# Kernel optimization log

Measured on AMD Instinct MI355X. Metric: run time of the kernel, lower is better.

The kernel has to match this reference:

```python
import jax, jax.numpy as jnp
import numpy as np

T, N, D, H = 128, 512, 1024, 1024
LN_EPS = 1e-5


def setup_inputs() -> dict:
    key = jax.random.key(0)
    ks = jax.random.split(key, 6)
    x = jax.random.normal(ks[0], (T * N, D), jnp.float32)
    hxs = jax.random.normal(ks[1], (N, 1, H), jnp.float32)
    # binary done-masks (float, mostly 1.0 = keep hidden state, 0.0 = episode reset)
    masks = (jax.random.uniform(ks[2], (T * N, 1)) < 0.95).astype(jnp.float32)
    s = 1.0 / np.sqrt(H)
    # PyTorch GRU packed gates, order (r, z, n): weight_ih_l0 [3H, D], weight_hh_l0 [3H, H]
    W_ih = jax.random.normal(ks[3], (3 * H, D), jnp.float32) * s
    W_hh = jax.random.normal(ks[4], (3 * H, H), jnp.float32) * s
    b_ih = jnp.zeros((3 * H,), jnp.float32)  # module inits biases to 0
    b_hh = jnp.zeros((3 * H,), jnp.float32)
    gamma = jnp.ones((H,), jnp.float32)
    beta = jnp.zeros((H,), jnp.float32)
    return dict(x=x, hxs=hxs, masks=masks, W_ih=W_ih, W_hh=W_hh,
                b_ih=b_ih, b_hh=b_hh, gamma=gamma, beta=beta)


def reference(x, hxs, masks, W_ih, W_hh, b_ih, b_hh, gamma, beta):
    TN = x.shape[0]
    Nn = hxs.shape[0]
    Tt = TN // Nn
    Hd = hxs.shape[-1]
    xs = x.reshape(Tt, Nn, -1)          # [T, N, D]
    m = masks.reshape(Tt, Nn)           # [T, N]
    # Chunk starts per source: t=0 plus every t>=1 where (masks[t] == 1).any().
    # At a chunk start the hidden state is multiplied by masks[t] (broadcast over layers);
    # a scan with a per-step conditional mask-multiply is exactly equivalent to the
    # torch loop over chunks.
    reset = jnp.concatenate([jnp.ones((1,), bool), jnp.any(m[1:] == 1.0, axis=-1)])
    # Batch the input projection across all T*N tokens (one big GEMM): [T, N, 3H]
    xp = jnp.einsum('tnd,gd->tng', xs, W_ih) + b_ih
    h0 = hxs[:, 0, :]                   # recurrent_N == 1 -> [N, H]

    def step(h, inp):
        xp_t, m_t, r_t = inp
        h = jnp.where(r_t, h * m_t[:, None], h)
        hp = h @ W_hh.T + b_hh          # [N, 3H]
        xr, xz, xn = jnp.split(xp_t, 3, axis=-1)
        hr, hz, hn = jnp.split(hp, 3, axis=-1)
        r = jax.nn.sigmoid(xr + hr)
        z = jax.nn.sigmoid(xz + hz)
        n = jnp.tanh(xn + r * hn)
        h_new = (1.0 - z) * n + z * h
        return h_new, h_new

    h_last, outs = jax.lax.scan(step, h0, (xp, m, reset))
    y = outs.reshape(Tt * Nn, Hd)
    # LayerNorm over last dim
    mu = y.mean(-1, keepdims=True)
    var = y.var(-1, keepdims=True)
    y = (y - mu) * jax.lax.rsqrt(var + LN_EPS) * gamma + beta
    return y, h_last[:, None, :]
```

## Files before the change

### kernel.cpp

```cpp
#include <hip/hip_runtime.h>

#define T_STEPS 128
#define N_B     512
#define D_IN    1024
#define H_DIM   1024
#define G_DIM   3072
#define M_ALL   (T_STEPS * N_B)

typedef short          s8v  __attribute__((ext_vector_type(8)));
typedef float          f4v  __attribute__((ext_vector_type(4)));
typedef unsigned short u4v  __attribute__((ext_vector_type(4)));

__device__ __forceinline__ unsigned short f2bf(float f) {
  union { float f; unsigned u; } v; v.f = f;
  unsigned r = v.u + 0x7FFFu + ((v.u >> 16) & 1u);
  return (unsigned short)(r >> 16);
}
__device__ __forceinline__ float bf2f(unsigned short h) {
  union { unsigned u; float f; } v; v.u = ((unsigned)h) << 16;
  return v.f;
}
__device__ __forceinline__ void async16(const void* g, void* l) {
  __builtin_amdgcn_global_load_lds(
      (const __attribute__((address_space(1))) unsigned*)g,
      (__attribute__((address_space(3))) unsigned*)l, 16, 0, 0);
}
__device__ __forceinline__ float sigmoidf_(float x) { return 1.f / (1.f + __expf(-x)); }
__device__ __forceinline__ float tanhf_(float x)    { return 1.f - 2.f / (1.f + __expf(2.f * x)); }

__global__ void cvt_bf16(const float* __restrict__ in, unsigned short* __restrict__ out, long n4) {
  long i = (long)blockIdx.x * blockDim.x + threadIdx.x;
  long stride = (long)gridDim.x * blockDim.x;
  for (; i < n4; i += stride) {
    f4v v = *(const f4v*)(in + i * 4);
    u4v o;
    #pragma unroll
    for (int e = 0; e < 4; ++e) o[e] = f2bf(v[e]);
    *(u4v*)(out + i * 4) = o;
  }
}

__global__ void reset_kernel(const float* __restrict__ masks, int* __restrict__ reset) {
  const int t = blockIdx.x;
  __shared__ int flag;
  if (threadIdx.x == 0) flag = (t == 0) ? 1 : 0;
  __syncthreads();
  if (t > 0 && masks[(size_t)t * N_B + threadIdx.x] == 1.0f) flag = 1;
  __syncthreads();
  if (threadIdx.x == 0) reset[t] = flag;
}

__global__ __launch_bounds__(256) void gemm_xp(const unsigned short* __restrict__ A,
                                               const unsigned short* __restrict__ B,
                                               const float* __restrict__ bias,
                                               unsigned short* __restrict__ C) {
  const int m0 = blockIdx.y * 128, g0 = blockIdx.x * 128;
  const int tid = threadIdx.x, wv = tid >> 6, l = tid & 63;
  const int l15 = l & 15, l4 = l >> 4;
  const int wr = wv >> 1, wc = wv & 1;
  __shared__ unsigned short As[128 * 64], Bs[128 * 64];

  f4v zero4 = {0.f, 0.f, 0.f, 0.f};
  f4v acc[4][4];
  #pragma unroll
  for (int i = 0; i < 4; ++i)
    #pragma unroll
    for (int j = 0; j < 4; ++j) acc[i][j] = zero4;

  const int srow = l >> 3;
  const int selem = ((l & 7) ^ srow) * 8;
  const int swz_rd = (l15 & 7) << 4;

  for (int kt = 0; kt < 1024; kt += 64) {
    #pragma unroll
    for (int cc = 0; cc < 4; ++cc) {
      int s = wv * 4 + cc;
      int row = s * 8 + srow;
      async16(A + (size_t)(m0 + row) * 1024 + kt + selem, &As[s * 512]);
      async16(B + (size_t)(g0 + row) * 1024 + kt + selem, &Bs[s * 512]);
    }
    __syncthreads();
    #pragma unroll
    for (int ks = 0; ks < 2; ++ks) {
      s8v a[4], b[4];
      #pragma unroll
      for (int i = 0; i < 4; ++i) {
        int ra = wr * 64 + i * 16 + l15, rb = wc * 64 + i * 16 + l15;
        int cb = (ks * 64 + l4 * 16) ^ swz_rd;
        a[i] = *(const s8v*)((const char*)As + ra * 128 + cb);
        b[i] = *(const s8v*)((const char*)Bs + rb * 128 + cb);
      }
      #pragma unroll
      for (int i = 0; i < 4; ++i)
        #pragma unroll
        for (int j = 0; j < 4; ++j)
          acc[i][j] = __builtin_amdgcn_mfma_f32_16x16x32_bf16(a[i], b[j], acc[i][j], 0, 0, 0);
    }
    __syncthreads();
  }
  #pragma unroll
  for (int j = 0; j < 4; ++j) {
    int gcol = g0 + wc * 64 + j * 16 + l15;
    float bv = bias[gcol];
    #pragma unroll
    for (int i = 0; i < 4; ++i) {
      int mrow = m0 + wr * 64 + i * 16 + l4 * 4;
      u4v o;
      #pragma unroll
      for (int r = 0; r < 4; ++r) o[r] = f2bf(acc[i][j][r] + bv);
      *(u4v*)(C + (size_t)gcol * M_ALL + mrow) = o;
    }
  }
}

__global__ __launch_bounds__(256) void gru_step7(
    const unsigned short* __restrict__ Whh,
    const unsigned short* __restrict__ xpT,
    const float* __restrict__ masks,
    const int* __restrict__ reset,
    const float* __restrict__ bhh,
    const float* __restrict__ hxs,
    const unsigned short* __restrict__ hread,
    unsigned short* __restrict__ hwrite,
    const float* __restrict__ hf32r,
    float* __restrict__ hf32w,
    float* __restrict__ y,
    float* __restrict__ hlast,
    int t) {
  const int bid = blockIdx.x;
  const int jt = bid & 31, nt = bid >> 5;
  const int j0 = jt * 32, n0 = nt * 64;
  const int tid = threadIdx.x, w = tid >> 6, l = tid & 63;
  const int l15 = l & 15, l4 = l >> 4;
  const int wn = w & 1, wj = w >> 1;
  const size_t NH = (size_t)N_B * H_DIM;

  __shared__ unsigned short Hs[3][64 * 128];
  __shared__ unsigned short Ws[3][96 * 128];
  __shared__ unsigned short xpl[3][32][64];

  const int lrow4 = l >> 4;
  const int lcb = (l & 15) * 16;
  const int swz_rd = (l15 & 7) << 4;

  const int jj = j0 + wj * 16 + l15;
  const int rst = reset[t];

  bool zo[2];
  #pragma unroll
  for (int i = 0; i < 2; ++i) {
    float mv = masks[(size_t)t * N_B + n0 + wn * 32 + i * 16 + l15];
    zo[i] = rst && (mv == 0.0f);
  }
  const float* hsrc = (t == 0) ? hxs : hf32r;
  float hreg[2][4], mreg[2][4];
  #pragma unroll
  for (int i = 0; i < 2; ++i)
    #pragma unroll
    for (int r = 0; r < 4; ++r) {
      const int n = n0 + wn * 32 + i * 16 + l4 * 4 + r;
      hreg[i][r] = hsrc[(size_t)n * H_DIM + jj];
      mreg[i][r] = masks[(size_t)t * N_B + n];
    }
  const float br = bhh[jj];
  const float bz = bhh[H_DIM + jj];
  const float bn = bhh[2 * H_DIM + jj];

  f4v zero4 = {0.f, 0.f, 0.f, 0.f};
  s8v zer8 = {0, 0, 0, 0, 0, 0, 0, 0};
  f4v acc[2][3];
  #pragma unroll
  for (int i = 0; i < 2; ++i)
    #pragma unroll
    for (int g3 = 0; g3 < 3; ++g3) acc[i][g3] = zero4;

  auto stage = [&](int buf, int kt) {
    #pragma unroll
    for (int q = 0; q < 4; ++q) {
      int rb = w * 16 + q * 4;
      int row = rb + lrow4;
      int cb = lcb ^ ((row & 7) << 4);
      async16(hread + (size_t)(n0 + row) * H_DIM + kt * 128 + (cb >> 1), &Hs[buf][rb * 128]);
    }
    #pragma unroll
    for (int q = 0; q < 6; ++q) {
      int rb = w * 24 + q * 4;
      int row = rb + lrow4;
      int gate = row >> 5, jjl = row & 31;
      int cb = lcb ^ ((row & 7) << 4);
      async16(Whh + ((size_t)gate * H_DIM + j0 + jjl) * H_DIM + kt * 128 + (cb >> 1),
              &Ws[buf][rb * 128]);
    }
  };

  stage(0, 0); stage(1, 1); stage(2, 2);

  {
    const int jl = w * 8 + (l >> 3);
    const int nelem = ((l & 7) ^ (l >> 3)) * 8;
    #pragma unroll
    for (int g3 = 0; g3 < 3; ++g3)
      async16(xpT + (size_t)(g3 * H_DIM + j0 + jl) * M_ALL + (size_t)t * N_B + n0 + nelem,
              &xpl[g3][w * 8][0]);
  }

#define KT_BODY(KT, VM, DO_STAGE)                                              \
  {                                                                            \
    asm volatile("s_waitcnt vmcnt(" #VM ")" ::: "memory");                     \
    __builtin_amdgcn_s_barrier();                                              \
    __builtin_amdgcn_sched_barrier(0);                                         \
    if (DO_STAGE) stage((KT + 2) % 3, KT + 2);                                 \
    const char* hb = (const char*)&Hs[KT % 3][0];                              \
    const char* wb = (const char*)&Ws[KT % 3][0];                              \
    _Pragma("unroll")                                                          \
    for (int ks = 0; ks < 4; ++ks) {                                           \
      const int kbb = (ks * 64 + l4 * 16) ^ swz_rd;                            \
      s8v a[2], b[3];                                                          \
      _Pragma("unroll")                                                        \
      for (int i = 0; i < 2; ++i) {                                            \
        a[i] = *(const s8v*)(hb + (wn * 32 + i * 16 + l15) * 256 + kbb);       \
        if (zo[i]) a[i] = zer8;                                                \
      }                                                                        \
      _Pragma("unroll")                                                        \
      for (int g3 = 0; g3 < 3; ++g3)                                           \
        b[g3] = *(const s8v*)(wb + (g3 * 32 + wj * 16 + l15) * 256 + kbb);     \
      _Pragma("unroll")                                                        \
      for (int i = 0; i < 2; ++i)                                              \
        _Pragma("unroll")                                                      \
        for (int g3 = 0; g3 < 3; ++g3)                                         \
          acc[i][g3] = __builtin_amdgcn_mfma_f32_16x16x32_bf16(a[i], b[g3],    \
                                                              acc[i][g3], 0, 0, 0); \
    }                                                                          \
  }

  KT_BODY(0, 23, false)
  KT_BODY(1, 13, true)
  KT_BODY(2, 13, true)
  KT_BODY(3, 10, true)
  KT_BODY(4, 10, true)
  KT_BODY(5, 10, true)
  KT_BODY(6, 10, false)
  KT_BODY(7, 0,  false)
#undef KT_BODY

  #pragma unroll
  for (int i = 0; i < 2; ++i) {
    #pragma unroll
    for (int r = 0; r < 4; ++r) {
      const int n = n0 + wn * 32 + i * 16 + l4 * 4 + r;
      const int nl = wn * 32 + i * 16 + l4 * 4 + r;
      const int jl = wj * 16 + l15;
      float hprev = hreg[i][r];
      if (rst && mreg[i][r] == 0.0f) hprev = 0.0f;
      const float hr = acc[i][0][r] + br;
      const float hz = acc[i][1][r] + bz;
      const float hn = acc[i][2][r] + bn;
      const char* xb = (const char*)&xpl[0][0][0];
      const int nb = (nl * 2) ^ ((jl & 7) << 4);
      const float xr = bf2f(*(const unsigned short*)(xb + 0 * 4096 + jl * 128 + nb));
      const float xz = bf2f(*(const unsigned short*)(xb + 1 * 4096 + jl * 128 + nb));
      const float xn = bf2f(*(const unsigned short*)(xb + 2 * 4096 + jl * 128 + nb));
      const float rg = sigmoidf_(xr + hr);
      const float zg = sigmoidf_(xz + hz);
      const float ng = tanhf_(xn + rg * hn);
      const float hnew = (1.f - zg) * ng + zg * hprev;
      const size_t gidx = (size_t)n * H_DIM + jj;
      y[(size_t)t * NH + gidx] = hnew;
      hwrite[gidx] = f2bf(hnew);
      hf32w[gidx] = hnew;
      if (t == T_STEPS - 1) hlast[gidx] = hnew;
    }
  }
}

__global__ __launch_bounds__(256) void ln_kernel(float* __restrict__ y,
                                                 const float* __restrict__ gamma,
                                                 const float* __restrict__ beta) {
  const size_t row = blockIdx.x;
  float* p = y + row * (size_t)H_DIM;
  const int tid = threadIdx.x;
  f4v v = *(const f4v*)(p + tid * 4);
  float s = v[0] + v[1] + v[2] + v[3];
  float q = v[0] * v[0] + v[1] * v[1] + v[2] * v[2] + v[3] * v[3];
  #pragma unroll
  for (int off = 32; off > 0; off >>= 1) {
    s += __shfl_down(s, off);
    q += __shfl_down(q, off);
  }
  __shared__ float sb[8];
  const int wid = tid >> 6, lid = tid & 63;
  if (lid == 0) { sb[wid] = s; sb[4 + wid] = q; }
  __syncthreads();
  float S = sb[0] + sb[1] + sb[2] + sb[3];
  float Q = sb[4] + sb[5] + sb[6] + sb[7];
  float mean = S * (1.f / H_DIM);
  float var = Q * (1.f / H_DIM) - mean * mean;
  float inv = rsqrtf(var + 1e-5f);
  f4v g4 = *(const f4v*)(gamma + tid * 4);
  f4v b4 = *(const f4v*)(beta + tid * 4);
  f4v o;
  #pragma unroll
  for (int e = 0; e < 4; ++e) o[e] = (v[e] - mean) * inv * g4[e] + b4[e];
  *(f4v*)(p + tid * 4) = o;
}

extern "C" void kernel_launch(void* const* d_in, const int* in_sizes, int n_in,
                              void* d_out, int out_size, void* d_ws, size_t ws_size,
                              hipStream_t stream) {
  const float* x     = (const float*)d_in[0];
  const float* hxs   = (const float*)d_in[1];
  const float* masks = (const float*)d_in[2];
  const float* W_ih  = (const float*)d_in[3];
  const float* W_hh  = (const float*)d_in[4];
  const float* b_ih  = (const float*)d_in[5];
  const float* b_hh  = (const float*)d_in[6];
  const float* gamma = (const float*)d_in[7];
  const float* beta  = (const float*)d_in[8];
  float* y = (float*)d_out;
  float* hlast = y + (size_t)T_STEPS * N_B * H_DIM;

  char* ws = (char*)d_ws;
  unsigned short* Wih_bf = (unsigned short*)ws;  ws += (size_t)G_DIM * D_IN * 2;
  unsigned short* Whh_bf = (unsigned short*)ws;  ws += (size_t)G_DIM * H_DIM * 2;
  unsigned short* xc_bf  = (unsigned short*)ws;  ws += (size_t)M_ALL * D_IN * 2;
  unsigned short* xpT_bf = (unsigned short*)ws;  ws += (size_t)G_DIM * M_ALL * 2;
  unsigned short* hbuf   = (unsigned short*)ws;  ws += (size_t)2 * N_B * H_DIM * 2;
  float* hf32            = (float*)ws;           ws += (size_t)2 * N_B * H_DIM * 4;
  int* reset             = (int*)ws;             ws += 512;

  cvt_bf16<<<1024, 256, 0, stream>>>(W_ih, Wih_bf, (long)G_DIM * D_IN / 4);
  cvt_bf16<<<1024, 256, 0, stream>>>(W_hh, Whh_bf, (long)G_DIM * H_DIM / 4);
  cvt_bf16<<<512, 256, 0, stream>>>(hxs, hbuf, (long)N_B * H_DIM / 4);
  reset_kernel<<<128, 512, 0, stream>>>(masks, reset);
  cvt_bf16<<<4096, 256, 0, stream>>>(x, xc_bf, (long)M_ALL * D_IN / 4);

  dim3 gg(G_DIM / 128, M_ALL / 128);
  gemm_xp<<<gg, 256, 0, stream>>>(xc_bf, Wih_bf, b_ih, xpT_bf);

  const size_t NH = (size_t)N_B * H_DIM;
  for (int t = 0; t < T_STEPS; ++t) {
    const unsigned short* hread = hbuf + (size_t)(t & 1) * NH;
    unsigned short* hwrite = hbuf + (size_t)((t & 1) ^ 1) * NH;
    const float* hf32r = hf32 + (size_t)(t & 1) * NH;
    float* hf32w = hf32 + (size_t)((t & 1) ^ 1) * NH;
    gru_step7<<<256, 256, 0, stream>>>(Whh_bf, xpT_bf, masks, reset, b_hh,
                                       hxs, hread, hwrite, hf32r, hf32w, y, hlast, t);
  }

  ln_kernel<<<T_STEPS * N_B, 256, 0, stream>>>(y, gamma, beta);
}
```

Baseline: 2.483 ms.

## Fuse GRU time steps into one persistent kernel with per-group grid barriers

Replaces the 128 per-timestep launches with a single persistent kernel that loops over time. Each block keeps its fp32 hidden slice in registers, and the blocks sharing a batch group synchronise through an atomic counter barrier. The aim is to remove per-step launch overhead and the fp32 hidden-state round trip through global memory. The kernel needs all 256 blocks to be co-resident, or the barrier can deadlock. The bf16 hidden loads use a cache-bypass flag so that other blocks' writes are visible, but the barrier uses relaxed atomics with no explicit fences, so cross-block ordering is a risk.

```diff
diff --git a/kernel.cpp b/kernel.cpp
--- a/kernel.cpp
+++ b/kernel.cpp
@@ -6,6 +6,7 @@
 #define H_DIM   1024
 #define G_DIM   3072
 #define M_ALL   (T_STEPS * N_B)
+#define BAR_STRIDE 64
 
 typedef short          s8v  __attribute__((ext_vector_type(8)));
 typedef float          f4v  __attribute__((ext_vector_type(4)));
@@ -24,6 +25,11 @@
   __builtin_amdgcn_global_load_lds(
       (const __attribute__((address_space(1))) unsigned*)g,
       (__attribute__((address_space(3))) unsigned*)l, 16, 0, 0);
+}
+__device__ __forceinline__ void async16_sc0(const void* g, void* l) {
+  __builtin_amdgcn_global_load_lds(
+      (const __attribute__((address_space(1))) unsigned*)g,
+      (__attribute__((address_space(3))) unsigned*)l, 16, 0, 1);
 }
 __device__ __forceinline__ float sigmoidf_(float x) { return 1.f / (1.f + __expf(-x)); }
 __device__ __forceinline__ float tanhf_(float x)    { return 1.f - 2.f / (1.f + __expf(2.f * x)); }
@@ -113,23 +119,20 @@
   }
 }
 
-__global__ __launch_bounds__(256) void gru_step7(
+__global__ __launch_bounds__(256) void rnn_chunk6(
     const unsigned short* __restrict__ Whh,
     const unsigned short* __restrict__ xpT,
     const float* __restrict__ masks,
     const int* __restrict__ reset,
     const float* __restrict__ bhh,
     const float* __restrict__ hxs,
-    const unsigned short* __restrict__ hread,
-    unsigned short* __restrict__ hwrite,
-    const float* __restrict__ hf32r,
-    float* __restrict__ hf32w,
+    unsigned short* hbuf,
     float* __restrict__ y,
     float* __restrict__ hlast,
-    int t) {
+    unsigned* bar) {
   const int bid = blockIdx.x;
-  const int jt = bid & 31, nt = bid >> 5;
-  const int j0 = jt * 32, n0 = nt * 64;
+  const int g = bid & 7, c = bid >> 3;
+  const int n0 = g * 64, j0 = c * 32;
   const int tid = threadIdx.x, w = tid >> 6, l = tid & 63;
   const int l15 = l & 15, l4 = l >> 4;
   const int wn = w & 1, wj = w >> 1;
@@ -144,132 +147,151 @@
   const int swz_rd = (l15 & 7) << 4;
 
   const int jj = j0 + wj * 16 + l15;
-  const int rst = reset[t];
-
-  bool zo[2];
-  #pragma unroll
-  for (int i = 0; i < 2; ++i) {
-    float mv = masks[(size_t)t * N_B + n0 + wn * 32 + i * 16 + l15];
-    zo[i] = rst && (mv == 0.0f);
-  }
-  const float* hsrc = (t == 0) ? hxs : hf32r;
-  float hreg[2][4], mreg[2][4];
-  #pragma unroll
-  for (int i = 0; i < 2; ++i)
-    #pragma unroll
-    for (int r = 0; r < 4; ++r) {
-      const int n = n0 + wn * 32 + i * 16 + l4 * 4 + r;
-      hreg[i][r] = hsrc[(size_t)n * H_DIM + jj];
-      mreg[i][r] = masks[(size_t)t * N_B + n];
-    }
   const float br = bhh[jj];
   const float bz = bhh[H_DIM + jj];
   const float bn = bhh[2 * H_DIM + jj];
 
+  float hreg[2][4];
+  #pragma unroll
+  for (int i = 0; i < 2; ++i)
+    #pragma unroll
+    for (int r = 0; r < 4; ++r)
+      hreg[i][r] = hxs[(size_t)(n0 + wn * 32 + i * 16 + l4 * 4 + r) * H_DIM + jj];
+
   f4v zero4 = {0.f, 0.f, 0.f, 0.f};
   s8v zer8 = {0, 0, 0, 0, 0, 0, 0, 0};
-  f4v acc[2][3];
-  #pragma unroll
-  for (int i = 0; i < 2; ++i)
-    #pragma unroll
-    for (int g3 = 0; g3 < 3; ++g3) acc[i][g3] = zero4;
-
-  auto stage = [&](int buf, int kt) {
-    #pragma unroll
-    for (int q = 0; q < 4; ++q) {
-      int rb = w * 16 + q * 4;
-      int row = rb + lrow4;
-      int cb = lcb ^ ((row & 7) << 4);
-      async16(hread + (size_t)(n0 + row) * H_DIM + kt * 128 + (cb >> 1), &Hs[buf][rb * 128]);
-    }
-    #pragma unroll
-    for (int q = 0; q < 6; ++q) {
-      int rb = w * 24 + q * 4;
-      int row = rb + lrow4;
-      int gate = row >> 5, jjl = row & 31;
-      int cb = lcb ^ ((row & 7) << 4);
-      async16(Whh + ((size_t)gate * H_DIM + j0 + jjl) * H_DIM + kt * 128 + (cb >> 1),
-              &Ws[buf][rb * 128]);
-    }
-  };
-
-  stage(0, 0); stage(1, 1); stage(2, 2);
-
-  {
-    const int jl = w * 8 + (l >> 3);
-    const int nelem = ((l & 7) ^ (l >> 3)) * 8;
-    #pragma unroll
-    for (int g3 = 0; g3 < 3; ++g3)
-      async16(xpT + (size_t)(g3 * H_DIM + j0 + jl) * M_ALL + (size_t)t * N_B + n0 + nelem,
-              &xpl[g3][w * 8][0]);
-  }
+
+  for (int t = 0; t < T_STEPS; ++t) {
+    const unsigned short* hread = hbuf + (size_t)(t & 1) * NH;
+    unsigned short* hwrite = hbuf + (size_t)((t & 1) ^ 1) * NH;
+    const int rst = reset[t];
+
+    bool zo[2];
+    #pragma unroll
+    for (int i = 0; i < 2; ++i) {
+      float mv = masks[(size_t)t * N_B + n0 + wn * 32 + i * 16 + l15];
+      zo[i] = rst && (mv == 0.0f);
+    }
+    float mreg[2][4];
+    #pragma unroll
+    for (int i = 0; i < 2; ++i)
+      #pragma unroll
+      for (int r = 0; r < 4; ++r)
+        mreg[i][r] = masks[(size_t)t * N_B + n0 + wn * 32 + i * 16 + l4 * 4 + r];
+
+    f4v acc[2][3];
+    #pragma unroll
+    for (int i = 0; i < 2; ++i)
+      #pragma unroll
+      for (int g3 = 0; g3 < 3; ++g3) acc[i][g3] = zero4;
+
+    auto stage = [&](int buf, int kt) {
+      #pragma unroll
+      for (int q = 0; q < 4; ++q) {
+        int rb = w * 16 + q * 4;
+        int row = rb + lrow4;
+        int cb = lcb ^ ((row & 7) << 4);
+        async16_sc0(hread + (size_t)(n0 + row) * H_DIM + kt * 128 + (cb >> 1),
+                    &Hs[buf][rb * 128]);
+      }
+      #pragma unroll
+      for (int q = 0; q < 6; ++q) {
+        int rb = w * 24 + q * 4;
+        int row = rb + lrow4;
+        int gate = row >> 5, jjl = row & 31;
+        int cb = lcb ^ ((row & 7) << 4);
+        async16(Whh + ((size_t)gate * H_DIM + j0 + jjl) * H_DIM + kt * 128 + (cb >> 1),
+                &Ws[buf][rb * 128]);
+      }
+    };
+
+    stage(0, 0); stage(1, 1); stage(2, 2);
+
+    {
+      const int jl = w * 8 + (l >> 3);
+      const int nelem = ((l & 7) ^ (l >> 3)) * 8;
+      #pragma unroll
+      for (int g3 = 0; g3 < 3; ++g3)
+        async16(xpT + (size_t)(g3 * H_DIM + j0 + jl) * M_ALL + (size_t)t * N_B + n0 + nelem,
+                &xpl[g3][w * 8][0]);
+    }
 
 #define KT_BODY(KT, VM, DO_STAGE)                                              \
-  {                                                                            \
-    asm volatile("s_waitcnt vmcnt(" #VM ")" ::: "memory");                     \
-    __builtin_amdgcn_s_barrier();                                              \
-    __builtin_amdgcn_sched_barrier(0);                                         \
-    if (DO_STAGE) stage((KT + 2) % 3, KT + 2);                                 \
-    const char* hb = (const char*)&Hs[KT % 3][0];                              \
-    const char* wb = (const char*)&Ws[KT % 3][0];                              \
-    _Pragma("unroll")                                                          \
-    for (int ks = 0; ks < 4; ++ks) {                                           \
-      const int kbb = (ks * 64 + l4 * 16) ^ swz_rd;                            \
-      s8v a[2], b[3];                                                          \
+    {                                                                          \
+      asm volatile("s_waitcnt vmcnt(" #VM ")" ::: "memory");                   \
+      __builtin_amdgcn_s_barrier();                                            \
+      __builtin_amdgcn_sched_barrier(0);                                       \
+      if (DO_STAGE) stage((KT + 2) % 3, KT + 2);                               \
+      const char* hb = (const char*)&Hs[KT % 3][0];                            \
+      const char* wb = (const char*)&Ws[KT % 3][0];                            \
       _Pragma("unroll")                                                        \
-      for (int i = 0; i < 2; ++i) {                                            \
-        a[i] = *(const s8v*)(hb + (wn * 32 + i * 16 + l15) * 256 + kbb);       \
-        if (zo[i]) a[i] = zer8;                                                \
-      }                                                                        \
-      _Pragma("unroll")                                                        \
-      for (int g3 = 0; g3 < 3; ++g3)                                           \
-        b[g3] = *(const s8v*)(wb + (g3 * 32 + wj * 16 + l15) * 256 + kbb);     \
-      _Pragma("unroll")                                                        \
-      for (int i = 0; i < 2; ++i)                                              \
+      for (int ks = 0; ks < 4; ++ks) {                                         \
+        const int kbb = (ks * 64 + l4 * 16) ^ swz_rd;                          \
+        s8v a[2], b[3];                                                        \
+        _Pragma("unroll")                                                      \
+        for (int i = 0; i < 2; ++i) {                                          \
+          a[i] = *(const s8v*)(hb + (wn * 32 + i * 16 + l15) * 256 + kbb);     \
+          if (zo[i]) a[i] = zer8;                                              \
+        }                                                                      \
         _Pragma("unroll")                                                      \
         for (int g3 = 0; g3 < 3; ++g3)                                         \
-          acc[i][g3] = __builtin_amdgcn_mfma_f32_16x16x32_bf16(a[i], b[g3],    \
-                                                              acc[i][g3], 0, 0, 0); \
-    }                                                                          \
-  }
-
-  KT_BODY(0, 23, false)
-  KT_BODY(1, 13, true)
-  KT_BODY(2, 13, true)
-  KT_BODY(3, 10, true)
-  KT_BODY(4, 10, true)
-  KT_BODY(5, 10, true)
-  KT_BODY(6, 10, false)
-  KT_BODY(7, 0,  false)
+          b[g3] = *(const s8v*)(wb + (g3 * 32 + wj * 16 + l15) * 256 + kbb);   \
+        _Pragma("unroll")                                                      \
+        for (int i = 0; i < 2; ++i)                                            \
+          _Pragma("unroll")                                                    \
+          for (int g3 = 0; g3 < 3; ++g3)                                       \
+            acc[i][g3] = __builtin_amdgcn_mfma_f32_16x16x32_bf16(a[i], b[g3],  \
+                                                                acc[i][g3], 0, 0, 0); \
+      }                                                                        \
+    }
+
+    KT_BODY(0, 23, false)
+    KT_BODY(1, 13, true)
+    KT_BODY(2, 13, true)
+    KT_BODY(3, 10, true)
+    KT_BODY(4, 10, true)
+    KT_BODY(5, 10, true)
+    KT_BODY(6, 10, false)
+    KT_BODY(7, 0,  false)
 #undef KT_BODY
 
-  #pragma unroll
-  for (int i = 0; i < 2; ++i) {
-    #pragma unroll
-    for (int r = 0; r < 4; ++r) {
-      const int n = n0 + wn * 32 + i * 16 + l4 * 4 + r;
-      const int nl = wn * 32 + i * 16 + l4 * 4 + r;
-      const int jl = wj * 16 + l15;
-      float hprev = hreg[i][r];
-      if (rst && mreg[i][r] == 0.0f) hprev = 0.0f;
-      const float hr = acc[i][0][r] + br;
-      const float hz = acc[i][1][r] + bz;
-      const float hn = acc[i][2][r] + bn;
-      const char* xb = (const char*)&xpl[0][0][0];
-      const int nb = (nl * 2) ^ ((jl & 7) << 4);
-      const float xr = bf2f(*(const unsigned short*)(xb + 0 * 4096 + jl * 128 + nb));
-      const float xz = bf2f(*(const unsigned short*)(xb + 1 * 4096 + jl * 128 + nb));
-      const float xn = bf2f(*(const unsigned short*)(xb + 2 * 4096 + jl * 128 + nb));
-      const float rg = sigmoidf_(xr + hr);
-      const float zg = sigmoidf_(xz + hz);
-      const float ng = tanhf_(xn + rg * hn);
-      const float hnew = (1.f - zg) * ng + zg * hprev;
-      const size_t gidx = (size_t)n * H_DIM + jj;
-      y[(size_t)t * NH + gidx] = hnew;
-      hwrite[gidx] = f2bf(hnew);
-      hf32w[gidx] = hnew;
-      if (t == T_STEPS - 1) hlast[gidx] = hnew;
-    }
+    #pragma unroll
+    for (int i = 0; i < 2; ++i) {
+      #pragma unroll
+      for (int r = 0; r < 4; ++r) {
+        const int n = n0 + wn * 32 + i * 16 + l4 * 4 + r;
+        const int nl = wn * 32 + i * 16 + l4 * 4 + r;
+        const int jl = wj * 16 + l15;
+        float hprev = hreg[i][r];
+        if (rst && mreg[i][r] == 0.0f) hprev = 0.0f;
+        const float hr = acc[i][0][r] + br;
+        const float hz = acc[i][1][r] + bz;
+        const float hn = acc[i][2][r] + bn;
+        const char* xb = (const char*)&xpl[0][0][0];
+        const int nb = (nl * 2) ^ ((jl & 7) << 4);
+        const float xr = bf2f(*(const unsigned short*)(xb + 0 * 4096 + jl * 128 + nb));
+        const float xz = bf2f(*(const unsigned short*)(xb + 1 * 4096 + jl * 128 + nb));
+        const float xn = bf2f(*(const unsigned short*)(xb + 2 * 4096 + jl * 128 + nb));
+        const float rg = sigmoidf_(xr + hr);
+        const float zg = sigmoidf_(xz + hz);
+        const float ng = tanhf_(xn + rg * hn);
+        const float hnew = (1.f - zg) * ng + zg * hprev;
+        hreg[i][r] = hnew;
+        const size_t gidx = (size_t)n * H_DIM + jj;
+        y[(size_t)t * NH + gidx] = hnew;
+        hwrite[gidx] = f2bf(hnew);
+        if (t == T_STEPS - 1) hlast[gidx] = hnew;
+      }
+    }
+
+    __syncthreads();
+    if (tid == 0) {
+      __hip_atomic_fetch_add(&bar[g * BAR_STRIDE], 1u, __ATOMIC_RELAXED, __HIP_MEMORY_SCOPE_AGENT);
+      const unsigned tgt = 32u * (unsigned)(t + 1);
+      while (__hip_atomic_load(&bar[g * BAR_STRIDE], __ATOMIC_RELAXED, __HIP_MEMORY_SCOPE_AGENT) < tgt)
+        __builtin_amdgcn_s_sleep(1);
+    }
+    __syncthreads();
   }
 }
 
@@ -325,9 +347,10 @@
   unsigned short* xc_bf  = (unsigned short*)ws;  ws += (size_t)M_ALL * D_IN * 2;
   unsigned short* xpT_bf = (unsigned short*)ws;  ws += (size_t)G_DIM * M_ALL * 2;
   unsigned short* hbuf   = (unsigned short*)ws;  ws += (size_t)2 * N_B * H_DIM * 2;
-  float* hf32            = (float*)ws;           ws += (size_t)2 * N_B * H_DIM * 4;
+  unsigned* bars         = (unsigned*)ws;        ws += 8 * BAR_STRIDE * sizeof(unsigned);
   int* reset             = (int*)ws;             ws += 512;
 
+  hipMemsetAsync(bars, 0, 8 * BAR_STRIDE * sizeof(unsigned), stream);
   cvt_bf16<<<1024, 256, 0, stream>>>(W_ih, Wih_bf, (long)G_DIM * D_IN / 4);
   cvt_bf16<<<1024, 256, 0, stream>>>(W_hh, Whh_bf, (long)G_DIM * H_DIM / 4);
   cvt_bf16<<<512, 256, 0, stream>>>(hxs, hbuf, (long)N_B * H_DIM / 4);
@@ -337,15 +360,8 @@
   dim3 gg(G_DIM / 128, M_ALL / 128);
   gemm_xp<<<gg, 256, 0, stream>>>(xc_bf, Wih_bf, b_ih, xpT_bf);
 
-  const size_t NH = (size_t)N_B * H_DIM;
-  for (int t = 0; t < T_STEPS; ++t) {
-    const unsigned short* hread = hbuf + (size_t)(t & 1) * NH;
-    unsigned short* hwrite = hbuf + (size_t)((t & 1) ^ 1) * NH;
-    const float* hf32r = hf32 + (size_t)(t & 1) * NH;
-    float* hf32w = hf32 + (size_t)((t & 1) ^ 1) * NH;
-    gru_step7<<<256, 256, 0, stream>>>(Whh_bf, xpT_bf, masks, reset, b_hh,
-                                       hxs, hread, hwrite, hf32r, hf32w, y, hlast, t);
-  }
+  rnn_chunk6<<<256, 256, 0, stream>>>(Whh_bf, xpT_bf, masks, reset, b_hh,
+                                      hxs, hbuf, y, hlast, bars);
 
   ln_kernel<<<T_STEPS * N_B, 256, 0, stream>>>(y, gamma, beta);
 }
```

Result: slower. 2.606 ms (+5.0%).
